# Performance work log

Measured on AMD Instinct MI355X. Metric: run time of the kernel, lower is better.

## Reference

```python
import jax, jax.numpy as jnp
import numpy as np
import math

DIM = 2880
N_HEADS = 64
N_KV = 8
HEAD_DIM = 64
WINDOW = 128          # layer_id = 0 (even) -> sliding window active
BASE = 150000.0
INIT_CTX = 4096
SCALE = 32.0
NTK_ALPHA = 1.0
NTK_BETA = 32.0
EPS = 1e-5
SEQ = 1536
BATCH = 1
SM_SCALE = 1.0 / math.sqrt(HEAD_DIM)


def _rope_tables(seq_len):
    """YaRN (NTK-by-parts) cos/sin tables, half-split convention. [S, D/2]."""
    freq = BASE ** (np.arange(0, HEAD_DIM, 2, dtype=np.float32) / HEAD_DIM)
    concentration = 0.1 * math.log(SCALE) + 1.0
    d_half = HEAD_DIM / 2
    low = d_half * math.log(INIT_CTX / (NTK_BETA * 2 * math.pi)) / math.log(BASE)
    high = d_half * math.log(INIT_CTX / (NTK_ALPHA * 2 * math.pi)) / math.log(BASE)
    interpolation = 1.0 / (SCALE * freq)
    extrapolation = 1.0 / freq
    ramp = (np.arange(d_half, dtype=np.float32) - low) / (high - low)
    mask = 1.0 - np.clip(ramp, 0.0, 1.0)
    inv_freq = interpolation * (1.0 - mask) + extrapolation * mask
    t = np.arange(seq_len, dtype=np.float32)
    freqs = np.outer(t, inv_freq)
    return (jnp.asarray(np.cos(freqs) * concentration),
            jnp.asarray(np.sin(freqs) * concentration))


def _apply_rope(x, cos, sin):
    # x: [B, S, H, D]; cos/sin: [S, D/2]
    c = cos[None, :, None, :]
    s = sin[None, :, None, :]
    x1, x2 = jnp.split(x, 2, axis=-1)
    return jnp.concatenate([x1 * c - x2 * s, x2 * c + x1 * s], axis=-1)


def setup_inputs() -> dict:
    key = jax.random.key(0)
    ks = jax.random.split(key, 5)
    x = jax.random.normal(ks[0], (BATCH, SEQ, DIM), dtype=jnp.float32)
    sinks = jax.random.normal(ks[1], (N_HEADS,), dtype=jnp.float32)
    norm_w = jnp.ones((DIM,), dtype=jnp.float32)
    qkv_dim = HEAD_DIM * (N_HEADS + 2 * N_KV)  # 5120
    qkv_w = jax.random.normal(ks[2], (qkv_dim, DIM), dtype=jnp.float32) / math.sqrt(DIM)
    qkv_b = jnp.zeros((qkv_dim,), dtype=jnp.float32)
    out_w = jax.random.normal(ks[3], (DIM, N_HEADS * HEAD_DIM), dtype=jnp.float32) / math.sqrt(N_HEADS * HEAD_DIM)
    out_b = jnp.zeros((DIM,), dtype=jnp.float32)
    return {"x": x, "sinks": sinks, "norm_w": norm_w, "qkv_w": qkv_w,
            "qkv_b": qkv_b, "out_w": out_w, "out_b": out_b}


def reference(x, sinks, norm_w, qkv_w, qkv_b, out_w, out_b):
    B, S, _ = x.shape
    # RMSNorm
    t = x * jax.lax.rsqrt(jnp.mean(x * x, axis=-1, keepdims=True) + EPS) * norm_w
    # fused QKV projection
    qkv = t @ qkv_w.T + qkv_b
    q_dim = N_HEADS * HEAD_DIM
    kv_dim = N_KV * HEAD_DIM
    q = qkv[..., :q_dim].reshape(B, S, N_HEADS, HEAD_DIM)
    k = qkv[..., q_dim:q_dim + kv_dim].reshape(B, S, N_KV, HEAD_DIM)
    v = qkv[..., q_dim + kv_dim:].reshape(B, S, N_KV, HEAD_DIM)
    # YaRN RoPE
    cos, sin = _rope_tables(S)
    q = _apply_rope(q, cos, sin)
    k = _apply_rope(k, cos, sin)
    # GQA: group query heads per kv head
    G = N_HEADS // N_KV
    qg = q.reshape(B, S, N_KV, G, HEAD_DIM)
    scores = jnp.einsum('bqkgd,bskd->bkgqs', qg, k) * SM_SCALE  # [B,KV,G,Sq,Sk]
    # causal + sliding-window mask
    i = jnp.arange(S)[:, None]
    j = jnp.arange(S)[None, :]
    allowed = j <= i
    if WINDOW > 0:
        allowed = allowed & ((i - j) < WINDOW)
    scores = jnp.where(allowed, scores, -jnp.inf)
    # sink tokens: one extra learned logit per head in the softmax denominator
    sink = sinks.reshape(N_KV, G)[None, :, :, None, None]
    sink = jnp.broadcast_to(sink, (B, N_KV, G, S, 1))
    logits = jnp.concatenate([scores, sink], axis=-1)  # [B,KV,G,Sq,Sk+1]
    p = jax.nn.softmax(logits, axis=-1)[..., :S]        # drop sink column
    attn = jnp.einsum('bkgqs,bskd->bqkgd', p, v).reshape(B, S, N_HEADS * HEAD_DIM)
    return attn @ out_w.T + out_b
```

## Files before the change

### kernel.cpp

```cpp
#include <hip/hip_runtime.h>

typedef unsigned short u16;
typedef unsigned int u32;
typedef __bf16 bf16x8 __attribute__((ext_vector_type(8)));
typedef float f32x4 __attribute__((ext_vector_type(4)));

#define S_LEN 1536
#define DIM 2880
#define NQH 64
#define NKVH 8
#define HD 64
#define QKV_N 5120
#define QDIM 4096
#define KVDIM 512
#define WIN 128
#define SM_SCALE 0.125f

__device__ __forceinline__ u16 f2bf(float f) {
  union { float f; u32 u; } a; a.f = f;
  u32 u = a.u;
  u32 lsb = (u >> 16) & 1;
  u += 0x7fffu + lsb;
  return (u16)(u >> 16);
}
__device__ __forceinline__ u32 pk2bf(float a, float b) {
  return (u32)f2bf(a) | ((u32)f2bf(b) << 16);
}

#define GLOAD16(g, l) __builtin_amdgcn_global_load_lds( \
    (const __attribute__((address_space(1))) u32*)(g), \
    (__attribute__((address_space(3))) u32*)(l), 16, 0, 0)

__global__ void rope_tables(float* __restrict__ cosT, float* __restrict__ sinT) {
  int idx = blockIdx.x * blockDim.x + threadIdx.x;
  if (idx >= S_LEN * 32) return;
  int s = idx >> 5, d = idx & 31;
  const double TWO_PI = 6.283185307179586;
  double freq = pow(150000.0, (double)d / 32.0);
  double conc = 0.1 * log(32.0) + 1.0;
  double lb = log(150000.0);
  double low = 32.0 * log(4096.0 / (32.0 * TWO_PI)) / lb;
  double high = 32.0 * log(4096.0 / (1.0 * TWO_PI)) / lb;
  double interp = 1.0 / (32.0 * freq), extra = 1.0 / freq;
  double ramp = ((double)d - low) / (high - low);
  ramp = ramp < 0.0 ? 0.0 : (ramp > 1.0 ? 1.0 : ramp);
  double maskv = 1.0 - ramp;
  double invf = interp * (1.0 - maskv) + extra * maskv;
  double ang = (double)s * invf;
  cosT[idx] = (float)(cos(ang) * conc);
  sinT[idx] = (float)(sin(ang) * conc);
}

__global__ __launch_bounds__(256) void rmsnorm_bf16(
    const float* __restrict__ x, const float* __restrict__ wgt,
    u16* __restrict__ th) {
  int row = blockIdx.x;
  const float* xr = x + (size_t)row * DIM;
  float ss = 0.f;
  for (int i = threadIdx.x; i < DIM / 4; i += 256) {
    float4 v = *(const float4*)&xr[i * 4];
    ss += v.x * v.x + v.y * v.y + v.z * v.z + v.w * v.w;
  }
  for (int m = 32; m >= 1; m >>= 1) ss += __shfl_xor(ss, m);
  __shared__ float red[4];
  int lane = threadIdx.x & 63, w = threadIdx.x >> 6;
  if (lane == 0) red[w] = ss;
  __syncthreads();
  float tot = red[0] + red[1] + red[2] + red[3];
  float scale = rsqrtf(tot / (float)DIM + 1e-5f);
  for (int i = threadIdx.x; i < DIM / 4; i += 256) {
    float4 v = *(const float4*)&xr[i * 4];
    float4 g = *(const float4*)&wgt[i * 4];
    ushort4 hi;
    hi.x = f2bf(v.x * scale * g.x);
    hi.y = f2bf(v.y * scale * g.y);
    hi.z = f2bf(v.z * scale * g.z);
    hi.w = f2bf(v.w * scale * g.w);
    *(ushort4*)&th[(size_t)row * DIM + i * 4] = hi;
  }
}

__global__ __launch_bounds__(256) void conv2(
    const float* __restrict__ s1, u16* __restrict__ d1, long n1,
    const float* __restrict__ s2, u16* __restrict__ d2, long n2) {
  long idx = (long)blockIdx.x * 256 + threadIdx.x;
  const float* src; u16* dst; long i;
  if (idx < n1) { src = s1; dst = d1; i = idx; }
  else if (idx < n1 + n2) { src = s2; dst = d2; i = idx - n1; }
  else return;
  float4 v = *(const float4*)&src[i * 4];
  ushort4 h;
  h.x = f2bf(v.x); h.y = f2bf(v.y); h.z = f2bf(v.z); h.w = f2bf(v.w);
  *(ushort4*)&dst[i * 4] = h;
}


__global__ __launch_bounds__(256, 3) void gemm_rope(
    const u16* __restrict__ A, const u16* __restrict__ B,
    const float* __restrict__ bias,
    const float* __restrict__ cosT, const float* __restrict__ sinT,
    u16* __restrict__ Qb, u16* __restrict__ Kb, u16* __restrict__ Vt) {
  __shared__ u16 As[3 * 4096];
  __shared__ u16 Bs[3 * 4096];
  const int K = DIM;
  const int t = threadIdx.x;
  const int lane = t & 63, w = t >> 6;

  const int nby = gridDim.y;
  const int nwg = gridDim.x * nby;
  int orig = blockIdx.x * nby + blockIdx.y;
  {
    int q = nwg >> 3, r = nwg & 7;
    int xcd = orig & 7, i = orig >> 3;
    orig = (xcd < r ? xcd * (q + 1) : r * (q + 1) + (xcd - r) * q) + i;
  }
  const int m0 = (orig % nby) * 128, n0 = (orig / nby) * 128;

  const int wr = (w >> 1) * 64, wc = (w & 1) * 64;
  const int lr = lane & 15, lk8 = (lane >> 4) * 8;
  const int lcol = lk8 ^ (((lr >> 1) & 3) << 3);
  const int g4 = (lane >> 4) * 4;
  f32x4 acc[4][4] = {};

  const int ks = ((t & 3) ^ ((t >> 3) & 3)) * 8;
  const size_t ga0 = (size_t)(m0 + (t >> 2)) * K + ks;
  const size_t ga1 = (size_t)(m0 + 64 + (t >> 2)) * K + ks;
  const size_t gb0 = (size_t)(n0 + (t >> 2)) * K + ks;
  const size_t gb1 = (size_t)(n0 + 64 + (t >> 2)) * K + ks;

  auto STAGE = [&](int buf, int k0) {
    GLOAD16(A + ga0 + k0, &As[buf * 4096 + t * 8]);
    GLOAD16(A + ga1 + k0, &As[buf * 4096 + (t + 256) * 8]);
    GLOAD16(B + gb0 + k0, &Bs[buf * 4096 + t * 8]);
    GLOAD16(B + gb1 + k0, &Bs[buf * 4096 + (t + 256) * 8]);
  };

  const int nk = K / 32;
  STAGE(0, 0); STAGE(1, 32);

  for (int tt = 0; tt < nk; ++tt) {
    const int cur = tt % 3;
    if (tt + 2 < nk) {
      STAGE((tt + 2) % 3, (tt + 2) * 32);
      asm volatile("s_waitcnt vmcnt(8)" ::: "memory");
    } else if (tt + 1 < nk) {
      asm volatile("s_waitcnt vmcnt(4)" ::: "memory");
    } else {
      asm volatile("s_waitcnt vmcnt(0)" ::: "memory");
    }
    __builtin_amdgcn_s_barrier();
    __builtin_amdgcn_sched_barrier(0);
    const u16* as_ = &As[cur * 4096];
    const u16* bs_ = &Bs[cur * 4096];
    bf16x8 af[4], bf_[4];
#pragma unroll
    for (int i = 0; i < 4; ++i) af[i] = *(const bf16x8*)&as_[(wr + i * 16 + lr) * 32 + lcol];
#pragma unroll
    for (int j = 0; j < 4; ++j) bf_[j] = *(const bf16x8*)&bs_[(wc + j * 16 + lr) * 32 + lcol];
    __builtin_amdgcn_s_setprio(1);
#pragma unroll
    for (int i = 0; i < 4; ++i)
#pragma unroll
      for (int j = 0; j < 4; ++j)
        acc[i][j] = __builtin_amdgcn_mfma_f32_16x16x32_bf16(af[i], bf_[j], acc[i][j], 0, 0, 0);
    __builtin_amdgcn_s_setprio(0);
    __builtin_amdgcn_sched_barrier(0);
    __builtin_amdgcn_s_barrier();
  }

  if (n0 < 4608) {
    const bool isQ = (n0 < 4096);
    const float sc = isQ ? SM_SCALE : 1.0f;
#pragma unroll
    for (int i = 0; i < 4; ++i) {
      const int row = m0 + wr + i * 16 + g4;
#pragma unroll
      for (int j = 0; j < 2; ++j) {
        const int col = n0 + wc + j * 16 + lr;
        const int d = j * 16 + lr;
        const float b1 = bias[col], b2 = bias[col + 32];
#pragma unroll
        for (int r = 0; r < 4; ++r) {
          const float c = cosT[(row + r) * 32 + d];
          const float s = sinT[(row + r) * 32 + d];
          const float x1 = acc[i][j][r] + b1;
          const float x2 = acc[i][j + 2][r] + b2;
          const float o1 = (x1 * c - x2 * s) * sc;
          const float o2 = (x2 * c + x1 * s) * sc;
          if (isQ) {
            Qb[(size_t)(row + r) * QDIM + col] = f2bf(o1);
            Qb[(size_t)(row + r) * QDIM + col + 32] = f2bf(o2);
          } else {
            Kb[(size_t)(row + r) * KVDIM + (col - 4096)] = f2bf(o1);
            Kb[(size_t)(row + r) * KVDIM + (col - 4096) + 32] = f2bf(o2);
          }
        }
      }
    }
  } else {
#pragma unroll
    for (int i = 0; i < 4; ++i) {
      const int rowb = m0 + wr + i * 16 + g4;
#pragma unroll
      for (int j = 0; j < 4; ++j) {
        const int col = n0 + wc + j * 16 + lr;
        const float bb = bias[col];
        ushort4 pk;
        pk.x = f2bf(acc[i][j][0] + bb);
        pk.y = f2bf(acc[i][j][1] + bb);
        pk.z = f2bf(acc[i][j][2] + bb);
        pk.w = f2bf(acc[i][j][3] + bb);
        *(ushort4*)&Vt[(size_t)(col - 4608) * S_LEN + rowb] = pk;
      }
    }
  }
}

__global__ __launch_bounds__(256, 3) void gemm_bt(
    const u16* __restrict__ A, const u16* __restrict__ B,
    const float* __restrict__ bias, float* __restrict__ C,
    int M, int N, int K) {
  __shared__ u16 As[3 * 4096];
  __shared__ u16 Bs[3 * 4096];
  const int t = threadIdx.x;
  const int lane = t & 63, w = t >> 6;

  const int nby = gridDim.y;
  const int nwg = gridDim.x * nby;
  int orig = blockIdx.x * nby + blockIdx.y;
  {
    int q = nwg >> 3, r = nwg & 7;
    int xcd = orig & 7, i = orig >> 3;
    orig = (xcd < r ? xcd * (q + 1) : r * (q + 1) + (xcd - r) * q) + i;
  }
  const int m0 = (orig % nby) * 128, n0 = (orig / nby) * 128;

  const int wr = (w >> 1) * 64, wc = (w & 1) * 64;
  const int lr = lane & 15, lk8 = (lane >> 4) * 8;
  const int lcol = lk8 ^ (((lr >> 1) & 3) << 3);
  const int g4 = (lane >> 4) * 4;
  f32x4 acc[4][4] = {};

  const int ks = ((t & 3) ^ ((t >> 3) & 3)) * 8;
  int rB0 = n0 + (t >> 2); if (rB0 > N - 1) rB0 = N - 1;
  int rB1 = n0 + 64 + (t >> 2); if (rB1 > N - 1) rB1 = N - 1;
  const size_t ga0 = (size_t)(m0 + (t >> 2)) * K + ks;
  const size_t ga1 = (size_t)(m0 + 64 + (t >> 2)) * K + ks;
  const size_t gb0 = (size_t)rB0 * K + ks;
  const size_t gb1 = (size_t)rB1 * K + ks;

  auto STAGE = [&](int buf, int k0) {
    GLOAD16(A + ga0 + k0, &As[buf * 4096 + t * 8]);
    GLOAD16(A + ga1 + k0, &As[buf * 4096 + (t + 256) * 8]);
    GLOAD16(B + gb0 + k0, &Bs[buf * 4096 + t * 8]);
    GLOAD16(B + gb1 + k0, &Bs[buf * 4096 + (t + 256) * 8]);
  };

  const int nk = K / 32;
  STAGE(0, 0); STAGE(1, 32);

  for (int tt = 0; tt < nk; ++tt) {
    const int cur = tt % 3;
    if (tt + 2 < nk) {
      STAGE((tt + 2) % 3, (tt + 2) * 32);
      asm volatile("s_waitcnt vmcnt(8)" ::: "memory");
    } else if (tt + 1 < nk) {
      asm volatile("s_waitcnt vmcnt(4)" ::: "memory");
    } else {
      asm volatile("s_waitcnt vmcnt(0)" ::: "memory");
    }
    __builtin_amdgcn_s_barrier();
    __builtin_amdgcn_sched_barrier(0);
    const u16* as_ = &As[cur * 4096];
    const u16* bs_ = &Bs[cur * 4096];
    bf16x8 af[4], bf_[4];
#pragma unroll
    for (int i = 0; i < 4; ++i) af[i] = *(const bf16x8*)&as_[(wr + i * 16 + lr) * 32 + lcol];
#pragma unroll
    for (int j = 0; j < 4; ++j) bf_[j] = *(const bf16x8*)&bs_[(wc + j * 16 + lr) * 32 + lcol];
    __builtin_amdgcn_s_setprio(1);
#pragma unroll
    for (int i = 0; i < 4; ++i)
#pragma unroll
      for (int j = 0; j < 4; ++j)
        acc[i][j] = __builtin_amdgcn_mfma_f32_16x16x32_bf16(af[i], bf_[j], acc[i][j], 0, 0, 0);
    __builtin_amdgcn_s_setprio(0);
    __builtin_amdgcn_sched_barrier(0);
    __builtin_amdgcn_s_barrier();
  }

#pragma unroll
  for (int i = 0; i < 4; ++i) {
    const int row = m0 + wr + i * 16 + g4;
#pragma unroll
    for (int j = 0; j < 4; ++j) {
      const int col = n0 + wc + j * 16 + lr;
      if (col < N) {
        const float bb = bias[col];
#pragma unroll
        for (int r = 0; r < 4; ++r)
          C[(size_t)(row + r) * N + col] = acc[i][j][r] + bb;
      }
    }
  }
}

__global__ __launch_bounds__(256) void attn2(
    const u16* __restrict__ Q, const u16* __restrict__ Kb, const u16* __restrict__ Vt,
    const float* __restrict__ sinks, u16* __restrict__ O) {
  const int h = blockIdx.x;
  const int kh = h >> 3;
  const int wid = threadIdx.x >> 6;
  const int lane = threadIdx.x & 63;
  const int q0 = blockIdx.y * 128 + wid * 32;
  const int lr = lane & 15;
  const int g = lane >> 4;

  bf16x8 bq[2][2];
#pragma unroll
  for (int qf = 0; qf < 2; ++qf)
#pragma unroll
    for (int kc = 0; kc < 2; ++kc)
      bq[qf][kc] = *(const bf16x8*)&Q[(size_t)(q0 + qf * 16 + lr) * QDIM + h * HD + kc * 32 + g * 8];

  f32x4 o[2][4] = {};
  float m_s[2] = {-1e30f, -1e30f};
  float l_s[2] = {0.f, 0.f};

  int js = q0 - 128; if (js < 0) js = 0;

  for (int j0 = js; j0 <= q0; j0 += 32) {
    bf16x8 ak[2][2];
#pragma unroll
    for (int jf = 0; jf < 2; ++jf)
#pragma unroll
      for (int kc = 0; kc < 2; ++kc)
        ak[jf][kc] = *(const bf16x8*)&Kb[(size_t)(j0 + jf * 16 + lr) * KVDIM + kh * HD + kc * 32 + g * 8];

    f32x4 st[2][2] = {};
#pragma unroll
    for (int jf = 0; jf < 2; ++jf)
#pragma unroll
      for (int qf = 0; qf < 2; ++qf) {
        st[jf][qf] = __builtin_amdgcn_mfma_f32_16x16x32_bf16(ak[jf][0], bq[qf][0], st[jf][qf], 0, 0, 0);
        st[jf][qf] = __builtin_amdgcn_mfma_f32_16x16x32_bf16(ak[jf][1], bq[qf][1], st[jf][qf], 0, 0, 0);
      }

    float pv[2][2][4];
    float tmax[2] = {-1e30f, -1e30f};
#pragma unroll
    for (int jf = 0; jf < 2; ++jf)
#pragma unroll
      for (int qf = 0; qf < 2; ++qf)
#pragma unroll
        for (int r = 0; r < 4; ++r) {
          int jv = j0 + jf * 16 + 4 * g + r;
          int qq = q0 + qf * 16 + lr;
          float sc = st[jf][qf][r];
          bool ok = (jv <= qq) && (qq - jv < WIN);
          sc = ok ? sc : -1e30f;
          pv[jf][qf][r] = sc;
          tmax[qf] = fmaxf(tmax[qf], sc);
        }
#pragma unroll
    for (int qf = 0; qf < 2; ++qf) {
      float tm = tmax[qf];
      tm = fmaxf(tm, __shfl_xor(tm, 16));
      tm = fmaxf(tm, __shfl_xor(tm, 32));
      const float mo = m_s[qf];
      const float mn = fmaxf(mo, tm);
      const float esc = __expf(mo - mn);
      float ps = 0.f;
#pragma unroll
      for (int jf = 0; jf < 2; ++jf)
#pragma unroll
        for (int r = 0; r < 4; ++r) {
          float sv = pv[jf][qf][r];
          float e = __expf(sv - mn);
          e = (sv <= -1e29f) ? 0.f : e;
          pv[jf][qf][r] = e;
          ps += e;
        }
      ps += __shfl_xor(ps, 16);
      ps += __shfl_xor(ps, 32);
      l_s[qf] = l_s[qf] * esc + ps;
      m_s[qf] = mn;
#pragma unroll
      for (int df = 0; df < 4; ++df) o[qf][df] *= esc;
    }

    bf16x8 pb[2];
    const int srcA = lr + ((g & 1) ? 32 : 0);
    const int srcB = srcA + 16;
    const bool hi_half = (g >= 2);
#pragma unroll
    for (int qf = 0; qf < 2; ++qf) {
      u32 w0a = pk2bf(pv[0][qf][0], pv[0][qf][1]);
      u32 w1a = pk2bf(pv[0][qf][2], pv[0][qf][3]);
      u32 w0b = pk2bf(pv[1][qf][0], pv[1][qf][1]);
      u32 w1b = pk2bf(pv[1][qf][2], pv[1][qf][3]);
      u32 a0 = (u32)__shfl((int)w0a, srcA, 64);
      u32 a1 = (u32)__shfl((int)w1a, srcA, 64);
      u32 a2 = (u32)__shfl((int)w0a, srcB, 64);
      u32 a3 = (u32)__shfl((int)w1a, srcB, 64);
      u32 b0 = (u32)__shfl((int)w0b, srcA, 64);
      u32 b1 = (u32)__shfl((int)w1b, srcA, 64);
      u32 b2 = (u32)__shfl((int)w0b, srcB, 64);
      u32 b3 = (u32)__shfl((int)w1b, srcB, 64);
      union { u32 d[4]; bf16x8 v; } u_;
      u_.d[0] = hi_half ? b0 : a0;
      u_.d[1] = hi_half ? b1 : a1;
      u_.d[2] = hi_half ? b2 : a2;
      u_.d[3] = hi_half ? b3 : a3;
      pb[qf] = u_.v;
    }

    bf16x8 av[4];
#pragma unroll
    for (int df = 0; df < 4; ++df)
      av[df] = *(const bf16x8*)&Vt[((size_t)kh * HD + df * 16 + lr) * S_LEN + j0 + g * 8];

#pragma unroll
    for (int qf = 0; qf < 2; ++qf)
#pragma unroll
      for (int df = 0; df < 4; ++df)
        o[qf][df] = __builtin_amdgcn_mfma_f32_16x16x32_bf16(av[df], pb[qf], o[qf][df], 0, 0, 0);
  }

  const float snk = sinks[h];
#pragma unroll
  for (int qf = 0; qf < 2; ++qf) {
    const float mo = m_s[qf];
    const float Mx = fmaxf(mo, snk);
    const float den = l_s[qf] * __expf(mo - Mx) + __expf(snk - Mx);
    const float osc = __expf(mo - Mx) / den;
    const int row = q0 + qf * 16 + lr;
#pragma unroll
    for (int df = 0; df < 4; ++df) {
      ushort4 pk;
      pk.x = f2bf(o[qf][df][0] * osc);
      pk.y = f2bf(o[qf][df][1] * osc);
      pk.z = f2bf(o[qf][df][2] * osc);
      pk.w = f2bf(o[qf][df][3] * osc);
      *(ushort4*)&O[(size_t)row * QDIM + h * HD + df * 16 + 4 * g] = pk;
    }
  }
}

extern "C" void kernel_launch(void* const* d_in, const int* in_sizes, int n_in,
                              void* d_out, int out_size, void* d_ws, size_t ws_size,
                              hipStream_t stream) {
  const float* x      = (const float*)d_in[0];
  const float* sinks  = (const float*)d_in[1];
  const float* norm_w = (const float*)d_in[2];
  const float* qkv_w  = (const float*)d_in[3];
  const float* qkv_b  = (const float*)d_in[4];
  const float* out_w  = (const float*)d_in[5];
  const float* out_b  = (const float*)d_in[6];
  float* out = (float*)d_out;

  char* ws = (char*)d_ws;
  size_t off = 0;
  auto take = [&](size_t bytes) -> void* {
    void* r = ws + off;
    off += (bytes + 255) & ~(size_t)255;
    return r;
  };
  float* cosT = (float*)take((size_t)S_LEN * 32 * 4);
  float* sinT = (float*)take((size_t)S_LEN * 32 * 4);
  u16* th  = (u16*)take((size_t)S_LEN * DIM * 2);
  u16* wh  = (u16*)take((size_t)QKV_N * DIM * 2);
  u16* ow  = (u16*)take((size_t)DIM * QDIM * 2);
  u16* Qb  = (u16*)take((size_t)S_LEN * QDIM * 2);
  u16* Kb  = (u16*)take((size_t)S_LEN * KVDIM * 2);
  u16* Vt  = (u16*)take((size_t)S_LEN * KVDIM * 2);
  u16* Ab  = (u16*)take((size_t)S_LEN * QDIM * 2);

  const long n1 = (long)QKV_N * DIM / 4;
  const long n2 = (long)DIM * QDIM / 4;

  rope_tables<<<(S_LEN * 32 + 255) / 256, 256, 0, stream>>>(cosT, sinT);
  rmsnorm_bf16<<<S_LEN, 256, 0, stream>>>(x, norm_w, th);
  conv2<<<(int)((n1 + n2 + 255) / 256), 256, 0, stream>>>(qkv_w, wh, n1, out_w, ow, n2);
  gemm_rope<<<dim3(QKV_N / 128, S_LEN / 128), 256, 0, stream>>>(
      th, wh, qkv_b, cosT, sinT, Qb, Kb, Vt);
  attn2<<<dim3(NQH, S_LEN / 128), 256, 0, stream>>>(Qb, Kb, Vt, sinks, Ab);
  gemm_bt<<<dim3((DIM + 127) / 128, (S_LEN + 127) / 128), 256, 0, stream>>>(
      Ab, ow, out_b, out, S_LEN, DIM, QDIM);
}
```

Baseline: 214.8 us.

## Fuse preprocessing kernels into one launch and retile output GEMM to 64x128

Merges the rope-table, RMSNorm and weight-conversion kernels into a single launch that dispatches on block index, removing two kernel launches and the gaps between them. The output projection GEMM moves from 128x128 tiles with a three-stage K=32 pipeline to 64x128 tiles with a double-buffered K=64 pipeline. This doubles the number of workgroups (23x24) so the GPU is better filled, at the cost of lower per-tile reuse and a shallower prefetch pipeline. The setprio hints are dropped.

```diff
diff --git a/kernel.cpp b/kernel.cpp
--- a/kernel.cpp
+++ b/kernel.cpp
@@ -16,6 +16,10 @@
 #define WIN 128
 #define SM_SCALE 0.125f
 
+#define CONV_BLOCKS 25920
+#define RMS_BLOCKS 1536
+#define ROPE_BLOCKS 192
+
 __device__ __forceinline__ u16 f2bf(float f) {
   union { float f; u32 u; } a; a.f = f;
   u32 u = a.u;
@@ -31,69 +35,70 @@
     (const __attribute__((address_space(1))) u32*)(g), \
     (__attribute__((address_space(3))) u32*)(l), 16, 0, 0)
 
-__global__ void rope_tables(float* __restrict__ cosT, float* __restrict__ sinT) {
-  int idx = blockIdx.x * blockDim.x + threadIdx.x;
-  if (idx >= S_LEN * 32) return;
-  int s = idx >> 5, d = idx & 31;
-  const double TWO_PI = 6.283185307179586;
-  double freq = pow(150000.0, (double)d / 32.0);
-  double conc = 0.1 * log(32.0) + 1.0;
-  double lb = log(150000.0);
-  double low = 32.0 * log(4096.0 / (32.0 * TWO_PI)) / lb;
-  double high = 32.0 * log(4096.0 / (1.0 * TWO_PI)) / lb;
-  double interp = 1.0 / (32.0 * freq), extra = 1.0 / freq;
-  double ramp = ((double)d - low) / (high - low);
-  ramp = ramp < 0.0 ? 0.0 : (ramp > 1.0 ? 1.0 : ramp);
-  double maskv = 1.0 - ramp;
-  double invf = interp * (1.0 - maskv) + extra * maskv;
-  double ang = (double)s * invf;
-  cosT[idx] = (float)(cos(ang) * conc);
-  sinT[idx] = (float)(sin(ang) * conc);
-}
-
-__global__ __launch_bounds__(256) void rmsnorm_bf16(
-    const float* __restrict__ x, const float* __restrict__ wgt,
-    u16* __restrict__ th) {
-  int row = blockIdx.x;
-  const float* xr = x + (size_t)row * DIM;
-  float ss = 0.f;
-  for (int i = threadIdx.x; i < DIM / 4; i += 256) {
-    float4 v = *(const float4*)&xr[i * 4];
-    ss += v.x * v.x + v.y * v.y + v.z * v.z + v.w * v.w;
-  }
-  for (int m = 32; m >= 1; m >>= 1) ss += __shfl_xor(ss, m);
-  __shared__ float red[4];
-  int lane = threadIdx.x & 63, w = threadIdx.x >> 6;
-  if (lane == 0) red[w] = ss;
-  __syncthreads();
-  float tot = red[0] + red[1] + red[2] + red[3];
-  float scale = rsqrtf(tot / (float)DIM + 1e-5f);
-  for (int i = threadIdx.x; i < DIM / 4; i += 256) {
-    float4 v = *(const float4*)&xr[i * 4];
-    float4 g = *(const float4*)&wgt[i * 4];
-    ushort4 hi;
-    hi.x = f2bf(v.x * scale * g.x);
-    hi.y = f2bf(v.y * scale * g.y);
-    hi.z = f2bf(v.z * scale * g.z);
-    hi.w = f2bf(v.w * scale * g.w);
-    *(ushort4*)&th[(size_t)row * DIM + i * 4] = hi;
-  }
-}
-
-__global__ __launch_bounds__(256) void conv2(
-    const float* __restrict__ s1, u16* __restrict__ d1, long n1,
-    const float* __restrict__ s2, u16* __restrict__ d2, long n2) {
-  long idx = (long)blockIdx.x * 256 + threadIdx.x;
-  const float* src; u16* dst; long i;
-  if (idx < n1) { src = s1; dst = d1; i = idx; }
-  else if (idx < n1 + n2) { src = s2; dst = d2; i = idx - n1; }
-  else return;
-  float4 v = *(const float4*)&src[i * 4];
-  ushort4 h;
-  h.x = f2bf(v.x); h.y = f2bf(v.y); h.z = f2bf(v.z); h.w = f2bf(v.w);
-  *(ushort4*)&dst[i * 4] = h;
-}
-
+__global__ __launch_bounds__(256) void pre_all(
+    const float* __restrict__ x, const float* __restrict__ norm_w,
+    u16* __restrict__ th,
+    const float* __restrict__ qkv_w, u16* __restrict__ wh,
+    const float* __restrict__ out_w, u16* __restrict__ ow,
+    float* __restrict__ cosT, float* __restrict__ sinT) {
+  const int b = blockIdx.x;
+  if (b < CONV_BLOCKS) {
+    const long n1 = (long)QKV_N * DIM / 4;
+    const long n2 = (long)DIM * QDIM / 4;
+    long idx = (long)b * 256 + threadIdx.x;
+    const float* src; u16* dst; long i;
+    if (idx < n1) { src = qkv_w; dst = wh; i = idx; }
+    else if (idx < n1 + n2) { src = out_w; dst = ow; i = idx - n1; }
+    else return;
+    float4 v = *(const float4*)&src[i * 4];
+    ushort4 h;
+    h.x = f2bf(v.x); h.y = f2bf(v.y); h.z = f2bf(v.z); h.w = f2bf(v.w);
+    *(ushort4*)&dst[i * 4] = h;
+  } else if (b < CONV_BLOCKS + RMS_BLOCKS) {
+    const int row = b - CONV_BLOCKS;
+    const float* xr = x + (size_t)row * DIM;
+    float ss = 0.f;
+    for (int i = threadIdx.x; i < DIM / 4; i += 256) {
+      float4 v = *(const float4*)&xr[i * 4];
+      ss += v.x * v.x + v.y * v.y + v.z * v.z + v.w * v.w;
+    }
+    for (int m = 32; m >= 1; m >>= 1) ss += __shfl_xor(ss, m);
+    __shared__ float red[4];
+    int lane = threadIdx.x & 63, w = threadIdx.x >> 6;
+    if (lane == 0) red[w] = ss;
+    __syncthreads();
+    float tot = red[0] + red[1] + red[2] + red[3];
+    float scale = rsqrtf(tot / (float)DIM + 1e-5f);
+    for (int i = threadIdx.x; i < DIM / 4; i += 256) {
+      float4 v = *(const float4*)&xr[i * 4];
+      float4 g = *(const float4*)&norm_w[i * 4];
+      ushort4 hi;
+      hi.x = f2bf(v.x * scale * g.x);
+      hi.y = f2bf(v.y * scale * g.y);
+      hi.z = f2bf(v.z * scale * g.z);
+      hi.w = f2bf(v.w * scale * g.w);
+      *(ushort4*)&th[(size_t)row * DIM + i * 4] = hi;
+    }
+  } else {
+    int idx = (b - CONV_BLOCKS - RMS_BLOCKS) * 256 + threadIdx.x;
+    if (idx >= S_LEN * 32) return;
+    int s = idx >> 5, d = idx & 31;
+    const double TWO_PI = 6.283185307179586;
+    double freq = pow(150000.0, (double)d / 32.0);
+    double conc = 0.1 * log(32.0) + 1.0;
+    double lb = log(150000.0);
+    double low = 32.0 * log(4096.0 / (32.0 * TWO_PI)) / lb;
+    double high = 32.0 * log(4096.0 / (1.0 * TWO_PI)) / lb;
+    double interp = 1.0 / (32.0 * freq), extra = 1.0 / freq;
+    double ramp = ((double)d - low) / (high - low);
+    ramp = ramp < 0.0 ? 0.0 : (ramp > 1.0 ? 1.0 : ramp);
+    double maskv = 1.0 - ramp;
+    double invf = interp * (1.0 - maskv) + extra * maskv;
+    double ang = (double)s * invf;
+    cosT[idx] = (float)(cos(ang) * conc);
+    sinT[idx] = (float)(sin(ang) * conc);
+  }
+}
 
 __global__ __launch_bounds__(256, 3) void gemm_rope(
     const u16* __restrict__ A, const u16* __restrict__ B,
@@ -220,8 +225,8 @@
     const u16* __restrict__ A, const u16* __restrict__ B,
     const float* __restrict__ bias, float* __restrict__ C,
     int M, int N, int K) {
-  __shared__ u16 As[3 * 4096];
-  __shared__ u16 Bs[3 * 4096];
+  __shared__ u16 As[2 * 4096];
+  __shared__ u16 Bs[2 * 8192];
   const int t = threadIdx.x;
   const int lane = t & 63, w = t >> 6;
 
@@ -233,64 +238,67 @@
     int xcd = orig & 7, i = orig >> 3;
     orig = (xcd < r ? xcd * (q + 1) : r * (q + 1) + (xcd - r) * q) + i;
   }
-  const int m0 = (orig % nby) * 128, n0 = (orig / nby) * 128;
-
-  const int wr = (w >> 1) * 64, wc = (w & 1) * 64;
+  const int m0 = (orig % nby) * 64, n0 = (orig / nby) * 128;
+
+  const int wr = (w >> 1) * 32, wc = (w & 1) * 64;
   const int lr = lane & 15, lk8 = (lane >> 4) * 8;
   const int lcol = lk8 ^ (((lr >> 1) & 3) << 3);
   const int g4 = (lane >> 4) * 4;
-  f32x4 acc[4][4] = {};
-
-  const int ks = ((t & 3) ^ ((t >> 3) & 3)) * 8;
+  f32x4 acc[2][4] = {};
+
   int rB0 = n0 + (t >> 2); if (rB0 > N - 1) rB0 = N - 1;
   int rB1 = n0 + 64 + (t >> 2); if (rB1 > N - 1) rB1 = N - 1;
-  const size_t ga0 = (size_t)(m0 + (t >> 2)) * K + ks;
-  const size_t ga1 = (size_t)(m0 + 64 + (t >> 2)) * K + ks;
-  const size_t gb0 = (size_t)rB0 * K + ks;
-  const size_t gb1 = (size_t)rB1 * K + ks;
+  const size_t ga  = (size_t)(m0 + (t >> 2)) * K + (((t & 3) ^ ((t >> 3) & 3)) * 8);
+  const size_t gb0 = (size_t)rB0 * K + (((t & 3) ^ ((t >> 3) & 3)) * 8);
+  const size_t gb1 = (size_t)rB1 * K + (((t & 3) ^ ((t >> 3) & 3)) * 8);
 
   auto STAGE = [&](int buf, int k0) {
-    GLOAD16(A + ga0 + k0, &As[buf * 4096 + t * 8]);
-    GLOAD16(A + ga1 + k0, &As[buf * 4096 + (t + 256) * 8]);
-    GLOAD16(B + gb0 + k0, &Bs[buf * 4096 + t * 8]);
-    GLOAD16(B + gb1 + k0, &Bs[buf * 4096 + (t + 256) * 8]);
+    GLOAD16(A + ga + k0,        &As[buf * 4096 + t * 8]);
+    GLOAD16(A + ga + k0 + 32,   &As[buf * 4096 + 2048 + t * 8]);
+    GLOAD16(B + gb0 + k0,       &Bs[buf * 8192 + t * 8]);
+    GLOAD16(B + gb1 + k0,       &Bs[buf * 8192 + (t + 256) * 8]);
+    GLOAD16(B + gb0 + k0 + 32,  &Bs[buf * 8192 + 4096 + t * 8]);
+    GLOAD16(B + gb1 + k0 + 32,  &Bs[buf * 8192 + 4096 + (t + 256) * 8]);
   };
 
-  const int nk = K / 32;
-  STAGE(0, 0); STAGE(1, 32);
-
-  for (int tt = 0; tt < nk; ++tt) {
-    const int cur = tt % 3;
-    if (tt + 2 < nk) {
-      STAGE((tt + 2) % 3, (tt + 2) * 32);
-      asm volatile("s_waitcnt vmcnt(8)" ::: "memory");
-    } else if (tt + 1 < nk) {
-      asm volatile("s_waitcnt vmcnt(4)" ::: "memory");
+  const int nk2 = K / 64;
+  STAGE(0, 0);
+
+  for (int tt = 0; tt < nk2; ++tt) {
+    const int cur = tt & 1;
+    if (tt + 1 < nk2) {
+      STAGE(cur ^ 1, (tt + 1) * 64);
+      asm volatile("s_waitcnt vmcnt(6)" ::: "memory");
     } else {
       asm volatile("s_waitcnt vmcnt(0)" ::: "memory");
     }
     __builtin_amdgcn_s_barrier();
     __builtin_amdgcn_sched_barrier(0);
     const u16* as_ = &As[cur * 4096];
-    const u16* bs_ = &Bs[cur * 4096];
-    bf16x8 af[4], bf_[4];
-#pragma unroll
-    for (int i = 0; i < 4; ++i) af[i] = *(const bf16x8*)&as_[(wr + i * 16 + lr) * 32 + lcol];
-#pragma unroll
-    for (int j = 0; j < 4; ++j) bf_[j] = *(const bf16x8*)&bs_[(wc + j * 16 + lr) * 32 + lcol];
-    __builtin_amdgcn_s_setprio(1);
-#pragma unroll
-    for (int i = 0; i < 4; ++i)
+    const u16* bs_ = &Bs[cur * 8192];
+    bf16x8 af[2][2], bf_[2][4];
+#pragma unroll
+    for (int ks = 0; ks < 2; ++ks) {
+#pragma unroll
+      for (int i = 0; i < 2; ++i)
+        af[ks][i] = *(const bf16x8*)&as_[ks * 2048 + (wr + i * 16 + lr) * 32 + lcol];
 #pragma unroll
       for (int j = 0; j < 4; ++j)
-        acc[i][j] = __builtin_amdgcn_mfma_f32_16x16x32_bf16(af[i], bf_[j], acc[i][j], 0, 0, 0);
-    __builtin_amdgcn_s_setprio(0);
+        bf_[ks][j] = *(const bf16x8*)&bs_[ks * 4096 + (wc + j * 16 + lr) * 32 + lcol];
+    }
+#pragma unroll
+    for (int ks = 0; ks < 2; ++ks)
+#pragma unroll
+      for (int i = 0; i < 2; ++i)
+#pragma unroll
+        for (int j = 0; j < 4; ++j)
+          acc[i][j] = __builtin_amdgcn_mfma_f32_16x16x32_bf16(af[ks][i], bf_[ks][j], acc[i][j], 0, 0, 0);
     __builtin_amdgcn_sched_barrier(0);
     __builtin_amdgcn_s_barrier();
   }
 
 #pragma unroll
-  for (int i = 0; i < 4; ++i) {
+  for (int i = 0; i < 2; ++i) {
     const int row = m0 + wr + i * 16 + g4;
 #pragma unroll
     for (int j = 0; j < 4; ++j) {
@@ -476,15 +484,11 @@
   u16* Vt  = (u16*)take((size_t)S_LEN * KVDIM * 2);
   u16* Ab  = (u16*)take((size_t)S_LEN * QDIM * 2);
 
-  const long n1 = (long)QKV_N * DIM / 4;
-  const long n2 = (long)DIM * QDIM / 4;
-
-  rope_tables<<<(S_LEN * 32 + 255) / 256, 256, 0, stream>>>(cosT, sinT);
-  rmsnorm_bf16<<<S_LEN, 256, 0, stream>>>(x, norm_w, th);
-  conv2<<<(int)((n1 + n2 + 255) / 256), 256, 0, stream>>>(qkv_w, wh, n1, out_w, ow, n2);
+  pre_all<<<CONV_BLOCKS + RMS_BLOCKS + ROPE_BLOCKS, 256, 0, stream>>>(
+      x, norm_w, th, qkv_w, wh, out_w, ow, cosT, sinT);
   gemm_rope<<<dim3(QKV_N / 128, S_LEN / 128), 256, 0, stream>>>(
       th, wh, qkv_b, cosT, sinT, Qb, Kb, Vt);
   attn2<<<dim3(NQH, S_LEN / 128), 256, 0, stream>>>(Qb, Kb, Vt, sinks, Ab);
-  gemm_bt<<<dim3((DIM + 127) / 128, (S_LEN + 127) / 128), 256, 0, stream>>>(
+  gemm_bt<<<dim3((DIM + 127) / 128, S_LEN / 64), 256, 0, stream>>>(
       Ab, ow, out_b, out, S_LEN, DIM, QDIM);
 }
```

Result: faster. 186.6 us (-13.1%).
